# Kernel tuning notes

Measured on AMD Instinct MI355X. Metric: run time of the kernel, lower is better.

The kernel has to match this reference:

```python
import jax, jax.numpy as jnp
import numpy as np

NUM_NODES = 100000
EMBED_DIM = 128
HIDDEN = 128
NUM_EDGES = 1600000


def gcn_conv(x, W, b, src, dst, num_nodes):
    """PyG GCNConv: x' = D^{-1/2} (A+I) D^{-1/2} (x W) + b, symmetric norm with self-loops."""
    x = x @ W  # [N, out]
    loops = jnp.arange(num_nodes, dtype=src.dtype)
    s = jnp.concatenate([src, loops])  # sources incl. self-loops
    d = jnp.concatenate([dst, loops])  # targets incl. self-loops
    deg = jax.ops.segment_sum(jnp.ones_like(d, dtype=x.dtype), d, num_segments=num_nodes)
    dis = jnp.where(deg > 0, jax.lax.rsqrt(deg), 0.0)  # deg^{-1/2}, 0 where isolated
    norm = dis[s] * dis[d]  # [E+N]
    msg = x[s] * norm[:, None]  # gather + scale
    out = jax.ops.segment_sum(msg, d, num_segments=num_nodes)  # scatter-add
    return out + b


def setup_inputs() -> dict:
    key = jax.random.key(0)
    k1, k2, k3, k4, k5, k6 = jax.random.split(key, 6)
    edge_index = jax.random.randint(k1, (2, NUM_EDGES), 0, NUM_NODES, dtype=jnp.int64)
    edge_attr = jax.random.normal(k2, (NUM_EDGES,), dtype=jnp.float32)
    emb = jax.random.normal(k3, (NUM_NODES, EMBED_DIM), dtype=jnp.float32) * 0.1
    W1 = jax.random.normal(k4, (EMBED_DIM, HIDDEN), dtype=jnp.float32) * (1.0 / np.sqrt(EMBED_DIM))
    b1 = jnp.zeros((HIDDEN,), dtype=jnp.float32)
    W2 = jax.random.normal(k5, (HIDDEN, HIDDEN), dtype=jnp.float32) * (1.0 / np.sqrt(HIDDEN))
    b2 = jnp.zeros((HIDDEN,), dtype=jnp.float32)
    return {"edge_index": edge_index, "edge_attr": edge_attr, "emb": emb,
            "W1": W1, "b1": b1, "W2": W2, "b2": b2}


def reference(edge_index, edge_attr, emb, W1, b1, W2, b2):
    src, dst = edge_index[0], edge_index[1]
    x = gcn_conv(emb, W1, b1, src, dst, NUM_NODES)
    x = jax.nn.relu(x)
    x = gcn_conv(x, W2, b2, src, dst, NUM_NODES)
    return x
```

## Files before the change

kernel.cpp:

```cpp
#include <hip/hip_runtime.h>

#define EMB 128
#define NBUC 1024
#define NPART 256
#define NSEG 8
#define SEGLEN (NPART / NSEG)

typedef __attribute__((ext_vector_type(8))) short short8;
typedef __attribute__((ext_vector_type(4))) float f32x4;
typedef __attribute__((ext_vector_type(2))) unsigned int uint2v;
typedef __attribute__((ext_vector_type(4))) float float4v;

__device__ __forceinline__ unsigned short f2bf(float f) {
    union { float f; unsigned int i; } v; v.f = f;
    unsigned int x = v.i;
    x += 0x7fffu + ((x >> 16) & 1u);
    return (unsigned short)(x >> 16);
}
__device__ __forceinline__ void acc_bf4(uint2 v, float& a0, float& a1, float& a2, float& a3) {
    union { unsigned int i; float f; } t;
    t.i = v.x << 16;          a0 += t.f;
    t.i = v.x & 0xffff0000u;  a1 += t.f;
    t.i = v.y << 16;          a2 += t.f;
    t.i = v.y & 0xffff0000u;  a3 += t.f;
}


__global__ __launch_bounds__(256) void p1_hist(const int* __restrict__ dst,
                                               int* __restrict__ BH, int E, int chunk) {
    __shared__ int h[NBUC];
    for (int i = threadIdx.x; i < NBUC; i += 256) h[i] = 0;
    __syncthreads();
    int s = blockIdx.x * chunk;
    int e = min(E, s + chunk);
    for (int i = s + threadIdx.x; i < e; i += 256)
        atomicAdd(&h[dst[i] >> 7], 1);
    __syncthreads();
    for (int i = threadIdx.x; i < NBUC; i += 256)
        BH[blockIdx.x * NBUC + i] = h[i];
}

__global__ __launch_bounds__(256) void p_segsum(const int* __restrict__ BH,
                                                int* __restrict__ SS) {
    int idx = blockIdx.x * 256 + threadIdx.x;
    int seg = idx >> 10, b = idx & (NBUC - 1);
    int s = 0;
#pragma unroll 8
    for (int k = 0; k < SEGLEN; ++k)
        s += BH[(seg * SEGLEN + k) * NBUC + b];
    SS[seg * NBUC + b] = s;
}

__global__ __launch_bounds__(1024) void p_scan(const int* __restrict__ SS,
                                               int* __restrict__ base, int E) {
    __shared__ int a[NBUC];
    int t = threadIdx.x;
    int v0 = 0;
#pragma unroll 8
    for (int s = 0; s < NSEG; ++s) v0 += SS[s * NBUC + t];
    a[t] = v0;
    __syncthreads();
    for (int off = 1; off < NBUC; off <<= 1) {
        int v = (t >= off) ? a[t - off] : 0;
        __syncthreads();
        a[t] += v;
        __syncthreads();
    }
    base[t] = a[t] - v0;
    if (t == NBUC - 1) base[NBUC] = E;
}

__global__ __launch_bounds__(256) void p_offs2(int* __restrict__ BH,
                                               const int* __restrict__ SS,
                                               const int* __restrict__ base) {
    int idx = blockIdx.x * 256 + threadIdx.x;
    int seg = idx >> 10, b = idx & (NBUC - 1);
    int run = base[b];
    for (int s = 0; s < seg; ++s) run += SS[s * NBUC + b];
#pragma unroll 4
    for (int k = 0; k < SEGLEN; ++k) {
        int* p = &BH[(seg * SEGLEN + k) * NBUC + b];
        int v = *p;
        *p = run;
        run += v;
    }
}

__global__ __launch_bounds__(256) void p2_scatter(const int* __restrict__ src,
                                                  const int* __restrict__ dst,
                                                  const int* __restrict__ BH,
                                                  int* __restrict__ part,
                                                  int E, int chunk) {
    __shared__ int cnt[NBUC];
    for (int i = threadIdx.x; i < NBUC; i += 256)
        cnt[i] = BH[blockIdx.x * NBUC + i];
    __syncthreads();
    int s = blockIdx.x * chunk;
    int e = min(E, s + chunk);
    for (int i = s + threadIdx.x; i < e; i += 256) {
        int d = dst[i];
        int pos = atomicAdd(&cnt[d >> 7], 1);
        part[pos] = src[i] | ((d & 127) << 17);
    }
}

__global__ __launch_bounds__(256) void p3_csr(const int* __restrict__ part,
                                              const int* __restrict__ base,
                                              int* __restrict__ R, int* __restrict__ adj,
                                              float* __restrict__ dis, int N, int E) {
    __shared__ int hist[128];
    __shared__ int sc[128];
    __shared__ int cnt[128];
    int b = blockIdx.x;
    int n0 = b * 128;
    int nn = min(128, N - n0);
    int s = base[b], e = base[b + 1];
    int t = threadIdx.x;

    if (t < 128) hist[t] = 0;
    __syncthreads();
    for (int i = s + t; i < e; i += 256)
        atomicAdd(&hist[part[i] >> 17], 1);
    __syncthreads();

    if (t < 128) sc[t] = hist[t];
    __syncthreads();
    for (int off = 1; off < 128; off <<= 1) {
        int v = 0;
        if (t < 128 && t >= off) v = sc[t - off];
        __syncthreads();
        if (t < 128) sc[t] += v;
        __syncthreads();
    }
    if (t < 128) {
        int excl = sc[t] - hist[t];
        cnt[t] = excl;
        if (t < nn) {
            R[n0 + t] = s + excl;
            dis[n0 + t] = rsqrtf((float)hist[t] + 1.0f);
        }
    }
    if (b == 0 && t == 0) R[N] = E;
    __syncthreads();

    for (int i = s + t; i < e; i += 256) {
        int p = part[i];
        int pos = atomicAdd(&cnt[p >> 17], 1);
        adj[s + pos] = p & 0x1FFFF;
    }
}

__global__ __launch_bounds__(256) void k_prep_w2(const float* __restrict__ W1,
                                                 const float* __restrict__ W2,
                                                 unsigned short* __restrict__ W1s,
                                                 unsigned short* __restrict__ W2s) {
    int gid = blockIdx.x * 256 + threadIdx.x;
    const float* W = (gid < 16384) ? W1 : W2;
    unsigned short* Ws = (gid < 16384) ? W1s : W2s;
    int idx = gid & 16383;
    int k = idx >> 7, n = idx & 127;
    int kk = k >> 5, q = (k >> 3) & 3, j = k & 7;
    int ct = n >> 4, nn = n & 15;
    int didx = ((((kk * 8 + ct) * 4 + q) * 16 + nn) << 3) + j;
    Ws[didx] = f2bf(W[idx]);
}

template <bool XBF16>
__global__ __launch_bounds__(256) void k_gemm_mfma(
    const void* Xv, const unsigned short* __restrict__ Wsw,
    const float* __restrict__ dis, unsigned short* Y, int N)
{
    __shared__ __align__(16) unsigned short lds[16384];

    {
        const uint4* srcp = (const uint4*)Wsw;
        uint4* dstp = (uint4*)lds;
        for (int i = threadIdx.x; i < 2048; i += 256) dstp[i] = srcp[i];
    }
    __syncthreads();

    const int wave = threadIdx.x >> 6;
    const int lane = threadIdx.x & 63;
    const int q = lane >> 4, nn = lane & 15;
    const int row0 = blockIdx.x * 64 + wave * 16;
    const int arow = row0 + nn;
    const int arc = arow < N ? arow : N - 1;

    f32x4 acc[8];
#pragma unroll
    for (int ct = 0; ct < 8; ++ct) acc[ct] = (f32x4){0.f, 0.f, 0.f, 0.f};

#pragma unroll
    for (int kk = 0; kk < 4; ++kk) {
        short8 af;
        if (XBF16) {
            af = *(const short8*)((const unsigned short*)Xv + (size_t)arc * EMB + kk * 32 + q * 8);
        } else {
            const float* xp = (const float*)Xv + (size_t)arc * EMB + kk * 32 + q * 8;
            float4 u0 = *(const float4*)xp;
            float4 u1 = *(const float4*)(xp + 4);
            af[0] = (short)f2bf(u0.x); af[1] = (short)f2bf(u0.y);
            af[2] = (short)f2bf(u0.z); af[3] = (short)f2bf(u0.w);
            af[4] = (short)f2bf(u1.x); af[5] = (short)f2bf(u1.y);
            af[6] = (short)f2bf(u1.z); af[7] = (short)f2bf(u1.w);
        }
#pragma unroll
        for (int ct = 0; ct < 8; ++ct) {
            short8 bf = ((const short8*)lds)[(kk * 8 + ct) * 64 + lane];
            acc[ct] = __builtin_amdgcn_mfma_f32_16x16x32_bf16(af, bf, acc[ct], 0, 0, 0);
        }
    }

    __syncthreads();

    float dv[4];
#pragma unroll
    for (int r = 0; r < 4; ++r) {
        int gm = row0 + q * 4 + r;
        dv[r] = dis[gm < N ? gm : N - 1];
    }
#pragma unroll
    for (int ct = 0; ct < 8; ++ct) {
#pragma unroll
        for (int r = 0; r < 4; ++r) {
            int ml = wave * 16 + q * 4 + r;
            lds[ml * 136 + ct * 16 + nn] = f2bf(acc[ct][r] * dv[r]);
        }
    }
    __syncthreads();

    const int rbase = blockIdx.x * 64;
    for (int i = threadIdx.x; i < 1024; i += 256) {
        int row = i >> 4, off = i & 15;
        int grow = rbase + row;
        if (grow < N) {
            uint4 v = *(const uint4*)(lds + row * 136 + off * 8);
            *((uint4*)(Y + (size_t)grow * EMB) + off) = v;
        }
    }
}

template <bool RELU, bool BF16OUT>
__global__ __launch_bounds__(256) void k_gather_finalize(
    const int* __restrict__ R, const int* __restrict__ adj,
    const unsigned short* __restrict__ Y, const float* __restrict__ dis,
    const float* __restrict__ bias, void* __restrict__ Outv, int N)
{
    int t = blockIdx.x * 256 + threadIdx.x;
    int n = t >> 5;
    if (n >= N) return;
    int j = (t & 31) * 4;

    int rs = R[n], re = R[n + 1];

    float a0 = 0.f, a1 = 0.f, a2 = 0.f, a3 = 0.f;
    uint2 sv = *(const uint2*)(Y + (size_t)n * EMB + j);
    acc_bf4(sv, a0, a1, a2, a3);

    int e = rs;
    for (; e + 3 < re; e += 4) {
        int s0 = __builtin_nontemporal_load(adj + e);
        int s1 = __builtin_nontemporal_load(adj + e + 1);
        int s2 = __builtin_nontemporal_load(adj + e + 2);
        int s3 = __builtin_nontemporal_load(adj + e + 3);
        uint2 v0 = *(const uint2*)(Y + (size_t)s0 * EMB + j);
        uint2 v1 = *(const uint2*)(Y + (size_t)s1 * EMB + j);
        uint2 v2 = *(const uint2*)(Y + (size_t)s2 * EMB + j);
        uint2 v3 = *(const uint2*)(Y + (size_t)s3 * EMB + j);
        acc_bf4(v0, a0, a1, a2, a3);
        acc_bf4(v1, a0, a1, a2, a3);
        acc_bf4(v2, a0, a1, a2, a3);
        acc_bf4(v3, a0, a1, a2, a3);
    }
    for (; e < re; ++e) {
        int s0 = __builtin_nontemporal_load(adj + e);
        uint2 v0 = *(const uint2*)(Y + (size_t)s0 * EMB + j);
        acc_bf4(v0, a0, a1, a2, a3);
    }

    float dv = dis[n];
    float4 b = *(const float4*)(bias + j);
    float o0 = dv * a0 + b.x;
    float o1 = dv * a1 + b.y;
    float o2 = dv * a2 + b.z;
    float o3 = dv * a3 + b.w;
    if (RELU) {
        o0 = fmaxf(o0, 0.f); o1 = fmaxf(o1, 0.f);
        o2 = fmaxf(o2, 0.f); o3 = fmaxf(o3, 0.f);
    }
    if (BF16OUT) {
        uint2v pk;
        pk.x = (unsigned)f2bf(o0) | ((unsigned)f2bf(o1) << 16);
        pk.y = (unsigned)f2bf(o2) | ((unsigned)f2bf(o3) << 16);
        __builtin_nontemporal_store(pk,
            (uint2v*)((unsigned short*)Outv + (size_t)n * EMB + j));
    } else {
        float4v o = { o0, o1, o2, o3 };
        __builtin_nontemporal_store(o,
            (float4v*)((float*)Outv + (size_t)n * EMB + j));
    }
}

extern "C" void kernel_launch(void* const* d_in, const int* in_sizes, int n_in,
                              void* d_out, int out_size, void* d_ws, size_t ws_size,
                              hipStream_t stream) {
    const int* ei = (const int*)d_in[0];
    const int E = in_sizes[0] / 2;
    const float* emb = (const float*)d_in[2];
    const int N = in_sizes[2] / EMB;
    const float* W1 = (const float*)d_in[3];
    const float* b1 = (const float*)d_in[4];
    const float* W2 = (const float*)d_in[5];
    const float* b2 = (const float*)d_in[6];
    float* out = (float*)d_out;

    const int* src = ei;
    const int* dstp = ei + E;

    char* w = (char*)d_ws;
    auto take = [&](size_t bytes) { char* p = w; w += (bytes + 511) & ~(size_t)511; return p; };
    float* dis  = (float*)take((size_t)N * 4);
    int*   R    = (int*)  take((size_t)(N + 1) * 4);
    int*   base = (int*)  take((size_t)(NBUC + 1) * 4);
    int*   SS   = (int*)  take((size_t)NSEG * NBUC * 4);
    int*   adj  = (int*)  take((size_t)E * 4);
    unsigned short* W1s = (unsigned short*)take((size_t)EMB * EMB * 2);
    unsigned short* W2s = (unsigned short*)take((size_t)EMB * EMB * 2);
    unsigned short* Hb  = (unsigned short*)take((size_t)N * EMB * 2);
    int*   part = (int*)Hb;
    int*   BH   = (int*)((char*)Hb + (((size_t)E * 4 + 511) & ~(size_t)511));
    unsigned short* Y1b = (unsigned short*)d_out;

    const int NB = (N + 127) / 128;
    const int chunk = (E + NPART - 1) / NPART;
    const int gM = (N + 63) / 64;
    const int gG = (N * 32 + 255) / 256;
    const int gS = (NSEG * NBUC) / 256;

    p1_hist   <<<NPART, 256, 0, stream>>>(dstp, BH, E, chunk);
    p_segsum  <<<gS, 256, 0, stream>>>(BH, SS);
    p_scan    <<<1, NBUC, 0, stream>>>(SS, base, E);
    p_offs2   <<<gS, 256, 0, stream>>>(BH, SS, base);
    p2_scatter<<<NPART, 256, 0, stream>>>(src, dstp, BH, part, E, chunk);
    p3_csr    <<<NB, 256, 0, stream>>>(part, base, R, adj, dis, N, E);

    k_prep_w2<<<128, 256, 0, stream>>>(W1, W2, W1s, W2s);

    k_gemm_mfma<false><<<gM, 256, 0, stream>>>(emb, W1s, dis, Y1b, N);
    k_gather_finalize<true, true><<<gG, 256, 0, stream>>>(R, adj, Y1b, dis, b1, Hb, N);

    k_gemm_mfma<true><<<gM, 256, 0, stream>>>(Hb, W2s, dis, Hb, N);
    k_gather_finalize<false, false><<<gG, 256, 0, stream>>>(R, adj, Hb, dis, b2, out, N);
}
```

Measured before the change: 348.8 us.

## Split features into per-XCD column slots and gather with work-stealing per slot

Intermediate Y/H buffers are stored column-sliced into 8 slots of 16 features (slot-major, 32 B per row). Each gather block reads its XCC_ID and starts on the matching slot. It pulls node chunks from an atomic per-slot counter, so one slot's working set (about 3.2 MB) stays resident in that XCD's L2. The goal is to cut cross-XCD L2 misses on the random neighbour gathers. The cost is that each edge's adjacency indices are re-read 8 times, and each gather touches only 4 bytes per lane.

```diff
diff --git a/kernel.cpp b/kernel.cpp
--- a/kernel.cpp
+++ b/kernel.cpp
@@ -5,11 +5,11 @@
 #define NPART 256
 #define NSEG 8
 #define SEGLEN (NPART / NSEG)
+#define NSLOT 8
+#define GCH 128
 
 typedef __attribute__((ext_vector_type(8))) short short8;
 typedef __attribute__((ext_vector_type(4))) float f32x4;
-typedef __attribute__((ext_vector_type(2))) unsigned int uint2v;
-typedef __attribute__((ext_vector_type(4))) float float4v;
 
 __device__ __forceinline__ unsigned short f2bf(float f) {
     union { float f; unsigned int i; } v; v.f = f;
@@ -17,12 +17,10 @@
     x += 0x7fffu + ((x >> 16) & 1u);
     return (unsigned short)(x >> 16);
 }
-__device__ __forceinline__ void acc_bf4(uint2 v, float& a0, float& a1, float& a2, float& a3) {
+__device__ __forceinline__ void acc_bf2(unsigned int v, float& a0, float& a1) {
     union { unsigned int i; float f; } t;
-    t.i = v.x << 16;          a0 += t.f;
-    t.i = v.x & 0xffff0000u;  a1 += t.f;
-    t.i = v.y << 16;          a2 += t.f;
-    t.i = v.y & 0xffff0000u;  a3 += t.f;
+    t.i = v << 16;          a0 += t.f;
+    t.i = v & 0xffff0000u;  a1 += t.f;
 }
 
 
@@ -153,8 +151,10 @@
 __global__ __launch_bounds__(256) void k_prep_w2(const float* __restrict__ W1,
                                                  const float* __restrict__ W2,
                                                  unsigned short* __restrict__ W1s,
-                                                 unsigned short* __restrict__ W2s) {
+                                                 unsigned short* __restrict__ W2s,
+                                                 int* __restrict__ ctr) {
     int gid = blockIdx.x * 256 + threadIdx.x;
+    if (blockIdx.x == 0 && threadIdx.x < 2 * NSLOT) ctr[threadIdx.x] = 0;
     const float* W = (gid < 16384) ? W1 : W2;
     unsigned short* Ws = (gid < 16384) ? W1s : W2s;
     int idx = gid & 16383;
@@ -194,7 +194,10 @@
     for (int kk = 0; kk < 4; ++kk) {
         short8 af;
         if (XBF16) {
-            af = *(const short8*)((const unsigned short*)Xv + (size_t)arc * EMB + kk * 32 + q * 8);
+            const int slot = kk * 2 + (q >> 1);
+            const int off = (q & 1) * 8;
+            af = *(const short8*)((const unsigned short*)Xv +
+                                  ((size_t)slot * N + arc) * 16 + off);
         } else {
             const float* xp = (const float*)Xv + (size_t)arc * EMB + kk * 32 + q * 8;
             float4 u0 = *(const float4*)xp;
@@ -231,73 +234,81 @@
 
     const int rbase = blockIdx.x * 64;
     for (int i = threadIdx.x; i < 1024; i += 256) {
-        int row = i >> 4, off = i & 15;
-        int grow = rbase + row;
+        int slot = i >> 7, r2 = (i >> 1) & 63, off = (i & 1) * 8;
+        int grow = rbase + r2;
         if (grow < N) {
-            uint4 v = *(const uint4*)(lds + row * 136 + off * 8);
-            *((uint4*)(Y + (size_t)grow * EMB) + off) = v;
+            uint4 v = *(const uint4*)(lds + r2 * 136 + slot * 16 + off);
+            *(uint4*)(Y + ((size_t)slot * N + grow) * 16 + off) = v;
         }
     }
 }
 
 template <bool RELU, bool BF16OUT>
-__global__ __launch_bounds__(256) void k_gather_finalize(
+__global__ __launch_bounds__(256) void k_gather_xcd(
     const int* __restrict__ R, const int* __restrict__ adj,
-    const unsigned short* __restrict__ Y, const float* __restrict__ dis,
-    const float* __restrict__ bias, void* __restrict__ Outv, int N)
+    const unsigned short* __restrict__ Yb, const float* __restrict__ dis,
+    const float* __restrict__ bias, void* __restrict__ Outv,
+    int* __restrict__ ctr, int N)
 {
-    int t = blockIdx.x * 256 + threadIdx.x;
-    int n = t >> 5;
-    if (n >= N) return;
-    int j = (t & 31) * 4;
-
-    int rs = R[n], re = R[n + 1];
-
-    float a0 = 0.f, a1 = 0.f, a2 = 0.f, a3 = 0.f;
-    uint2 sv = *(const uint2*)(Y + (size_t)n * EMB + j);
-    acc_bf4(sv, a0, a1, a2, a3);
-
-    int e = rs;
-    for (; e + 3 < re; e += 4) {
-        int s0 = __builtin_nontemporal_load(adj + e);
-        int s1 = __builtin_nontemporal_load(adj + e + 1);
-        int s2 = __builtin_nontemporal_load(adj + e + 2);
-        int s3 = __builtin_nontemporal_load(adj + e + 3);
-        uint2 v0 = *(const uint2*)(Y + (size_t)s0 * EMB + j);
-        uint2 v1 = *(const uint2*)(Y + (size_t)s1 * EMB + j);
-        uint2 v2 = *(const uint2*)(Y + (size_t)s2 * EMB + j);
-        uint2 v3 = *(const uint2*)(Y + (size_t)s3 * EMB + j);
-        acc_bf4(v0, a0, a1, a2, a3);
-        acc_bf4(v1, a0, a1, a2, a3);
-        acc_bf4(v2, a0, a1, a2, a3);
-        acc_bf4(v3, a0, a1, a2, a3);
-    }
-    for (; e < re; ++e) {
-        int s0 = __builtin_nontemporal_load(adj + e);
-        uint2 v0 = *(const uint2*)(Y + (size_t)s0 * EMB + j);
-        acc_bf4(v0, a0, a1, a2, a3);
-    }
-
-    float dv = dis[n];
-    float4 b = *(const float4*)(bias + j);
-    float o0 = dv * a0 + b.x;
-    float o1 = dv * a1 + b.y;
-    float o2 = dv * a2 + b.z;
-    float o3 = dv * a3 + b.w;
-    if (RELU) {
-        o0 = fmaxf(o0, 0.f); o1 = fmaxf(o1, 0.f);
-        o2 = fmaxf(o2, 0.f); o3 = fmaxf(o3, 0.f);
-    }
-    if (BF16OUT) {
-        uint2v pk;
-        pk.x = (unsigned)f2bf(o0) | ((unsigned)f2bf(o1) << 16);
-        pk.y = (unsigned)f2bf(o2) | ((unsigned)f2bf(o3) << 16);
-        __builtin_nontemporal_store(pk,
-            (uint2v*)((unsigned short*)Outv + (size_t)n * EMB + j));
-    } else {
-        float4v o = { o0, o1, o2, o3 };
-        __builtin_nontemporal_store(o,
-            (float4v*)((float*)Outv + (size_t)n * EMB + j));
+    __shared__ int scur;
+    int xcc;
+    asm volatile("s_getreg_b32 %0, hwreg(HW_REG_XCC_ID)" : "=s"(xcc));
+    xcc &= (NSLOT - 1);
+    const int g = threadIdx.x >> 3;
+    const int l = threadIdx.x & 7;
+    const int NCH = (N + GCH - 1) / GCH;
+
+    for (int soff = 0; soff < NSLOT; ++soff) {
+        const int slot = (xcc + soff) & (NSLOT - 1);
+        const unsigned int* __restrict__ Ysu =
+            (const unsigned int*)(Yb + (size_t)slot * N * 16);
+        const float bl0 = bias[slot * 16 + l * 2];
+        const float bl1 = bias[slot * 16 + l * 2 + 1];
+        for (;;) {
+            if (threadIdx.x == 0) scur = atomicAdd(&ctr[slot], 1);
+            __syncthreads();
+            const int c = scur;
+            __syncthreads();
+            if (c >= NCH) break;
+            const int n0 = c * GCH;
+#pragma unroll
+            for (int p = 0; p < GCH / 32; ++p) {
+                const int n = n0 + p * 32 + g;
+                if (n >= N) continue;
+                float a0, a1;
+                {
+                    unsigned int v = Ysu[n * 8 + l];
+                    union { unsigned int i; float f; } t;
+                    t.i = v << 16;         a0 = t.f;
+                    t.i = v & 0xffff0000u; a1 = t.f;
+                }
+                int e = R[n];
+                const int re = R[n + 1];
+                for (; e + 3 < re; e += 4) {
+                    int s0 = adj[e], s1 = adj[e + 1], s2 = adj[e + 2], s3 = adj[e + 3];
+                    unsigned int v0 = Ysu[s0 * 8 + l];
+                    unsigned int v1 = Ysu[s1 * 8 + l];
+                    unsigned int v2 = Ysu[s2 * 8 + l];
+                    unsigned int v3 = Ysu[s3 * 8 + l];
+                    acc_bf2(v0, a0, a1); acc_bf2(v1, a0, a1);
+                    acc_bf2(v2, a0, a1); acc_bf2(v3, a0, a1);
+                }
+                for (; e < re; ++e) {
+                    acc_bf2(Ysu[adj[e] * 8 + l], a0, a1);
+                }
+                const float dv = dis[n];
+                float o0 = dv * a0 + bl0;
+                float o1 = dv * a1 + bl1;
+                if (RELU) { o0 = fmaxf(o0, 0.f); o1 = fmaxf(o1, 0.f); }
+                if (BF16OUT) {
+                    unsigned int pk = (unsigned)f2bf(o0) | ((unsigned)f2bf(o1) << 16);
+                    ((unsigned int*)Outv)[(size_t)slot * N * 8 + n * 8 + l] = pk;
+                } else {
+                    float2 o = { o0, o1 };
+                    *(float2*)((float*)Outv + (size_t)n * EMB + slot * 16 + l * 2) = o;
+                }
+            }
+        }
     }
 }
 
@@ -323,6 +334,7 @@
     int*   R    = (int*)  take((size_t)(N + 1) * 4);
     int*   base = (int*)  take((size_t)(NBUC + 1) * 4);
     int*   SS   = (int*)  take((size_t)NSEG * NBUC * 4);
+    int*   ctr  = (int*)  take((size_t)2 * NSLOT * 4);
     int*   adj  = (int*)  take((size_t)E * 4);
     unsigned short* W1s = (unsigned short*)take((size_t)EMB * EMB * 2);
     unsigned short* W2s = (unsigned short*)take((size_t)EMB * EMB * 2);
@@ -334,7 +346,7 @@
     const int NB = (N + 127) / 128;
     const int chunk = (E + NPART - 1) / NPART;
     const int gM = (N + 63) / 64;
-    const int gG = (N * 32 + 255) / 256;
+    const int gG = 2048;
     const int gS = (NSEG * NBUC) / 256;
 
     p1_hist   <<<NPART, 256, 0, stream>>>(dstp, BH, E, chunk);
@@ -344,11 +356,11 @@
     p2_scatter<<<NPART, 256, 0, stream>>>(src, dstp, BH, part, E, chunk);
     p3_csr    <<<NB, 256, 0, stream>>>(part, base, R, adj, dis, N, E);
 
-    k_prep_w2<<<128, 256, 0, stream>>>(W1, W2, W1s, W2s);
+    k_prep_w2<<<128, 256, 0, stream>>>(W1, W2, W1s, W2s, ctr);
 
     k_gemm_mfma<false><<<gM, 256, 0, stream>>>(emb, W1s, dis, Y1b, N);
-    k_gather_finalize<true, true><<<gG, 256, 0, stream>>>(R, adj, Y1b, dis, b1, Hb, N);
+    k_gather_xcd<true, true><<<gG, 256, 0, stream>>>(R, adj, Y1b, dis, b1, Hb, ctr, N);
 
     k_gemm_mfma<true><<<gM, 256, 0, stream>>>(Hb, W2s, dis, Hb, N);
-    k_gather_finalize<false, false><<<gG, 256, 0, stream>>>(R, adj, Hb, dis, b2, out, N);
-}
+    k_gather_xcd<false, false><<<gG, 256, 0, stream>>>(R, adj, Hb, dis, b2, out, ctr + NSLOT, N);
+}
```

After: 808.5 us. 2.32x slower.

## Fuse CSR build stages with weight prep and GEMM1 by moving source norm to gather

Applied to the files above, without the earlier changes.

Moves the per-source degree normalisation out of the GEMM and into the gather loop, which now loads dis[src] per edge. Because the first GEMM no longer depends on dis, it is fused into the same launch as the edge scatter. Weight preparation is merged into the histogram launch. Nontemporal loads and stores in the gather are replaced by plain ones. This cuts launches and serialization between stages, at the cost of an extra random dis lookup per edge in both gathers.

```diff
diff --git a/kernel.cpp b/kernel.cpp
--- a/kernel.cpp
+++ b/kernel.cpp
@@ -5,11 +5,10 @@
 #define NPART 256
 #define NSEG 8
 #define SEGLEN (NPART / NSEG)
+#define PREPB 128
 
 typedef __attribute__((ext_vector_type(8))) short short8;
 typedef __attribute__((ext_vector_type(4))) float f32x4;
-typedef __attribute__((ext_vector_type(2))) unsigned int uint2v;
-typedef __attribute__((ext_vector_type(4))) float float4v;
 
 __device__ __forceinline__ unsigned short f2bf(float f) {
     union { float f; unsigned int i; } v; v.f = f;
@@ -17,27 +16,54 @@
     x += 0x7fffu + ((x >> 16) & 1u);
     return (unsigned short)(x >> 16);
 }
-__device__ __forceinline__ void acc_bf4(uint2 v, float& a0, float& a1, float& a2, float& a3) {
+__device__ __forceinline__ void acc_fma4(uint2 v, float d,
+                                         float& a0, float& a1, float& a2, float& a3) {
     union { unsigned int i; float f; } t;
-    t.i = v.x << 16;          a0 += t.f;
-    t.i = v.x & 0xffff0000u;  a1 += t.f;
-    t.i = v.y << 16;          a2 += t.f;
-    t.i = v.y & 0xffff0000u;  a3 += t.f;
-}
-
-
-__global__ __launch_bounds__(256) void p1_hist(const int* __restrict__ dst,
-                                               int* __restrict__ BH, int E, int chunk) {
-    __shared__ int h[NBUC];
+    t.i = v.x << 16;          a0 = fmaf(d, t.f, a0);
+    t.i = v.x & 0xffff0000u;  a1 = fmaf(d, t.f, a1);
+    t.i = v.y << 16;          a2 = fmaf(d, t.f, a2);
+    t.i = v.y & 0xffff0000u;  a3 = fmaf(d, t.f, a3);
+}
+
+
+__device__ __forceinline__ void p1_body(int bid, int* h, const int* __restrict__ dst,
+                                        int* __restrict__ BH, int E, int chunk) {
     for (int i = threadIdx.x; i < NBUC; i += 256) h[i] = 0;
     __syncthreads();
-    int s = blockIdx.x * chunk;
+    int s = bid * chunk;
     int e = min(E, s + chunk);
     for (int i = s + threadIdx.x; i < e; i += 256)
         atomicAdd(&h[dst[i] >> 7], 1);
     __syncthreads();
     for (int i = threadIdx.x; i < NBUC; i += 256)
-        BH[blockIdx.x * NBUC + i] = h[i];
+        BH[bid * NBUC + i] = h[i];
+}
+
+__device__ __forceinline__ void prepw_body(int bid, const float* __restrict__ W1,
+                                           const float* __restrict__ W2,
+                                           unsigned short* __restrict__ W1s,
+                                           unsigned short* __restrict__ W2s) {
+    int gid = bid * 256 + threadIdx.x;
+    const float* W = (gid < 16384) ? W1 : W2;
+    unsigned short* Ws = (gid < 16384) ? W1s : W2s;
+    int idx = gid & 16383;
+    int k = idx >> 7, n = idx & 127;
+    int kk = k >> 5, q = (k >> 3) & 3, j = k & 7;
+    int ct = n >> 4, nn = n & 15;
+    int didx = ((((kk * 8 + ct) * 4 + q) * 16 + nn) << 3) + j;
+    Ws[didx] = f2bf(W[idx]);
+}
+
+__global__ __launch_bounds__(256) void k_start(const int* __restrict__ dst,
+                                               int* __restrict__ BH, int E, int chunk,
+                                               const float* __restrict__ W1,
+                                               const float* __restrict__ W2,
+                                               unsigned short* __restrict__ W1s,
+                                               unsigned short* __restrict__ W2s) {
+    __shared__ int h[NBUC];
+    int b = blockIdx.x;
+    if (b < NPART) p1_body(b, h, dst, BH, E, chunk);
+    else           prepw_body(b - NPART, W1, W2, W1s, W2s);
 }
 
 __global__ __launch_bounds__(256) void p_segsum(const int* __restrict__ BH,
@@ -86,16 +112,16 @@
     }
 }
 
-__global__ __launch_bounds__(256) void p2_scatter(const int* __restrict__ src,
-                                                  const int* __restrict__ dst,
-                                                  const int* __restrict__ BH,
-                                                  int* __restrict__ part,
-                                                  int E, int chunk) {
-    __shared__ int cnt[NBUC];
+__device__ __forceinline__ void scatter_body(int bid, int* cnt,
+                                             const int* __restrict__ src,
+                                             const int* __restrict__ dst,
+                                             const int* __restrict__ BH,
+                                             int* __restrict__ part,
+                                             int E, int chunk) {
     for (int i = threadIdx.x; i < NBUC; i += 256)
-        cnt[i] = BH[blockIdx.x * NBUC + i];
-    __syncthreads();
-    int s = blockIdx.x * chunk;
+        cnt[i] = BH[bid * NBUC + i];
+    __syncthreads();
+    int s = bid * chunk;
     int e = min(E, s + chunk);
     for (int i = s + threadIdx.x; i < e; i += 256) {
         int d = dst[i];
@@ -150,28 +176,11 @@
     }
 }
 
-__global__ __launch_bounds__(256) void k_prep_w2(const float* __restrict__ W1,
-                                                 const float* __restrict__ W2,
-                                                 unsigned short* __restrict__ W1s,
-                                                 unsigned short* __restrict__ W2s) {
-    int gid = blockIdx.x * 256 + threadIdx.x;
-    const float* W = (gid < 16384) ? W1 : W2;
-    unsigned short* Ws = (gid < 16384) ? W1s : W2s;
-    int idx = gid & 16383;
-    int k = idx >> 7, n = idx & 127;
-    int kk = k >> 5, q = (k >> 3) & 3, j = k & 7;
-    int ct = n >> 4, nn = n & 15;
-    int didx = ((((kk * 8 + ct) * 4 + q) * 16 + nn) << 3) + j;
-    Ws[didx] = f2bf(W[idx]);
-}
-
 template <bool XBF16>
-__global__ __launch_bounds__(256) void k_gemm_mfma(
+__device__ __forceinline__ void gemm_body(int bid, unsigned short* lds,
     const void* Xv, const unsigned short* __restrict__ Wsw,
-    const float* __restrict__ dis, unsigned short* Y, int N)
+    unsigned short* __restrict__ Y, int N)
 {
-    __shared__ __align__(16) unsigned short lds[16384];
-
     {
         const uint4* srcp = (const uint4*)Wsw;
         uint4* dstp = (uint4*)lds;
@@ -182,7 +191,7 @@
     const int wave = threadIdx.x >> 6;
     const int lane = threadIdx.x & 63;
     const int q = lane >> 4, nn = lane & 15;
-    const int row0 = blockIdx.x * 64 + wave * 16;
+    const int row0 = bid * 64 + wave * 16;
     const int arow = row0 + nn;
     const int arc = arow < N ? arow : N - 1;
 
@@ -213,23 +222,17 @@
 
     __syncthreads();
 
-    float dv[4];
-#pragma unroll
-    for (int r = 0; r < 4; ++r) {
-        int gm = row0 + q * 4 + r;
-        dv[r] = dis[gm < N ? gm : N - 1];
-    }
 #pragma unroll
     for (int ct = 0; ct < 8; ++ct) {
 #pragma unroll
         for (int r = 0; r < 4; ++r) {
             int ml = wave * 16 + q * 4 + r;
-            lds[ml * 136 + ct * 16 + nn] = f2bf(acc[ct][r] * dv[r]);
-        }
-    }
-    __syncthreads();
-
-    const int rbase = blockIdx.x * 64;
+            lds[ml * 136 + ct * 16 + nn] = f2bf(acc[ct][r]);
+        }
+    }
+    __syncthreads();
+
+    const int rbase = bid * 64;
     for (int i = threadIdx.x; i < 1024; i += 256) {
         int row = i >> 4, off = i & 15;
         int grow = rbase + row;
@@ -238,6 +241,26 @@
             *((uint4*)(Y + (size_t)grow * EMB) + off) = v;
         }
     }
+}
+
+__global__ __launch_bounds__(256) void k_mid(
+    const int* __restrict__ src, const int* __restrict__ dstp,
+    const int* __restrict__ BH, int* __restrict__ part, int E, int chunk,
+    const void* Xv, const unsigned short* __restrict__ W1s,
+    unsigned short* __restrict__ Y, int N)
+{
+    __shared__ __align__(16) unsigned short smem[16384];
+    int b = blockIdx.x;
+    if (b < NPART) scatter_body(b, (int*)smem, src, dstp, BH, part, E, chunk);
+    else           gemm_body<false>(b - NPART, smem, Xv, W1s, Y, N);
+}
+
+__global__ __launch_bounds__(256) void k_gemm2(
+    const void* Xv, const unsigned short* __restrict__ Wsw,
+    unsigned short* __restrict__ Y, int N)
+{
+    __shared__ __align__(16) unsigned short smem[16384];
+    gemm_body<true>(blockIdx.x, smem, Xv, Wsw, Y, N);
 }
 
 template <bool RELU, bool BF16OUT>
@@ -252,33 +275,32 @@
     int j = (t & 31) * 4;
 
     int rs = R[n], re = R[n + 1];
+    float dv = dis[n];
 
     float a0 = 0.f, a1 = 0.f, a2 = 0.f, a3 = 0.f;
     uint2 sv = *(const uint2*)(Y + (size_t)n * EMB + j);
-    acc_bf4(sv, a0, a1, a2, a3);
+    acc_fma4(sv, dv, a0, a1, a2, a3);
 
     int e = rs;
     for (; e + 3 < re; e += 4) {
-        int s0 = __builtin_nontemporal_load(adj + e);
-        int s1 = __builtin_nontemporal_load(adj + e + 1);
-        int s2 = __builtin_nontemporal_load(adj + e + 2);
-        int s3 = __builtin_nontemporal_load(adj + e + 3);
+        int s0 = adj[e], s1 = adj[e + 1], s2 = adj[e + 2], s3 = adj[e + 3];
+        float d0 = dis[s0], d1 = dis[s1], d2 = dis[s2], d3 = dis[s3];
         uint2 v0 = *(const uint2*)(Y + (size_t)s0 * EMB + j);
         uint2 v1 = *(const uint2*)(Y + (size_t)s1 * EMB + j);
         uint2 v2 = *(const uint2*)(Y + (size_t)s2 * EMB + j);
         uint2 v3 = *(const uint2*)(Y + (size_t)s3 * EMB + j);
-        acc_bf4(v0, a0, a1, a2, a3);
-        acc_bf4(v1, a0, a1, a2, a3);
-        acc_bf4(v2, a0, a1, a2, a3);
-        acc_bf4(v3, a0, a1, a2, a3);
+        acc_fma4(v0, d0, a0, a1, a2, a3);
+        acc_fma4(v1, d1, a0, a1, a2, a3);
+        acc_fma4(v2, d2, a0, a1, a2, a3);
+        acc_fma4(v3, d3, a0, a1, a2, a3);
     }
     for (; e < re; ++e) {
-        int s0 = __builtin_nontemporal_load(adj + e);
+        int s0 = adj[e];
+        float d0 = dis[s0];
         uint2 v0 = *(const uint2*)(Y + (size_t)s0 * EMB + j);
-        acc_bf4(v0, a0, a1, a2, a3);
-    }
-
-    float dv = dis[n];
+        acc_fma4(v0, d0, a0, a1, a2, a3);
+    }
+
     float4 b = *(const float4*)(bias + j);
     float o0 = dv * a0 + b.x;
     float o1 = dv * a1 + b.y;
@@ -289,15 +311,11 @@
         o2 = fmaxf(o2, 0.f); o3 = fmaxf(o3, 0.f);
     }
     if (BF16OUT) {
-        uint2v pk;
-        pk.x = (unsigned)f2bf(o0) | ((unsigned)f2bf(o1) << 16);
-        pk.y = (unsigned)f2bf(o2) | ((unsigned)f2bf(o3) << 16);
-        __builtin_nontemporal_store(pk,
-            (uint2v*)((unsigned short*)Outv + (size_t)n * EMB + j));
+        ushort4 o = { f2bf(o0), f2bf(o1), f2bf(o2), f2bf(o3) };
+        *(ushort4*)((unsigned short*)Outv + (size_t)n * EMB + j) = o;
     } else {
-        float4v o = { o0, o1, o2, o3 };
-        __builtin_nontemporal_store(o,
-            (float4v*)((float*)Outv + (size_t)n * EMB + j));
+        float4 o = { o0, o1, o2, o3 };
+        *(float4*)((float*)Outv + (size_t)n * EMB + j) = o;
     }
 }
 
@@ -337,18 +355,17 @@
     const int gG = (N * 32 + 255) / 256;
     const int gS = (NSEG * NBUC) / 256;
 
-    p1_hist   <<<NPART, 256, 0, stream>>>(dstp, BH, E, chunk);
+    k_start   <<<NPART + PREPB, 256, 0, stream>>>(dstp, BH, E, chunk, W1, W2, W1s, W2s);
     p_segsum  <<<gS, 256, 0, stream>>>(BH, SS);
     p_scan    <<<1, NBUC, 0, stream>>>(SS, base, E);
     p_offs2   <<<gS, 256, 0, stream>>>(BH, SS, base);
-    p2_scatter<<<NPART, 256, 0, stream>>>(src, dstp, BH, part, E, chunk);
+
+    k_mid     <<<NPART + gM, 256, 0, stream>>>(src, dstp, BH, part, E, chunk,
+                                               emb, W1s, Y1b, N);
     p3_csr    <<<NB, 256, 0, stream>>>(part, base, R, adj, dis, N, E);
 
-    k_prep_w2<<<128, 256, 0, stream>>>(W1, W2, W1s, W2s);
-
-    k_gemm_mfma<false><<<gM, 256, 0, stream>>>(emb, W1s, dis, Y1b, N);
     k_gather_finalize<true, true><<<gG, 256, 0, stream>>>(R, adj, Y1b, dis, b1, Hb, N);
 
-    k_gemm_mfma<true><<<gM, 256, 0, stream>>>(Hb, W2s, dis, Hb, N);
+    k_gemm2<<<gM, 256, 0, stream>>>(Hb, W2s, Hb, N);
     k_gather_finalize<false, false><<<gG, 256, 0, stream>>>(R, adj, Hb, dis, b2, out, N);
 }
```

Measured after the change: 327.7 us. 6.1% less time.
